# Kernel tuning notes

Hardware: AMD Instinct MI355X
Metric: run time of the kernel (lower is better)

The kernel has to match this reference:

```python
import jax, jax.numpy as jnp
import numpy as np

FEATURE_LIST = [10, 13, 13, 7, 3, 6, 3, 13, 5, 4, 6, 4, 5, 4, 4, 5, 4, 3, 3, 7, 3, 3]
BATCH = 1048576
D_IN = sum(FEATURE_LIST)  # 128


def setup_inputs() -> dict:
    key = jax.random.key(0)
    k1, k2, k3 = jax.random.split(key, 3)
    x = jax.random.normal(k1, (BATCH, D_IN), dtype=jnp.float32)
    # per-block kernels (fn, 1) packed along axis 0 into (128, 1); 'uniform' init
    kernels = jax.random.uniform(k2, (D_IN, 1), dtype=jnp.float32, minval=-0.05, maxval=0.05)
    biases = jnp.zeros((len(FEATURE_LIST),), dtype=jnp.float32)
    final_kernel = jax.random.uniform(k3, (len(FEATURE_LIST), 1), dtype=jnp.float32, minval=-0.05, maxval=0.05)
    final_bias = jnp.zeros((1,), dtype=jnp.float32)
    return {"x": x, "kernels": kernels, "biases": biases,
            "final_kernel": final_kernel, "final_bias": final_bias}


def reference(x, kernels, biases, final_kernel, final_bias):
    nodes = []
    off = 0
    start_i = 0  # NOTE: original TF code never increments start_i -> every block reads x[:, 0:fn]
    for i, fn in enumerate(FEATURE_LIST):
        k = kernels[off:off + fn]                      # (fn, 1)
        node = jax.nn.relu(x[:, start_i:start_i + fn] @ k + biases[i])  # (B, 1)
        nodes.append(node)
        off += fn
    h = jnp.concatenate(nodes, axis=1)                 # (B, 22)
    return jax.nn.sigmoid(h @ final_kernel + final_bias)  # (B, 1)
```

## Files before the change

### kernel.cpp

```cpp
#include <hip/hip_runtime.h>
#include <math.h>

#define NFEAT 22
#define ROWS_PER_THREAD 2
#define BLOCK 256


__global__ __launch_bounds__(BLOCK, 8) void hnn_fused_kernel(
    const float* __restrict__ x,
    const float* __restrict__ kernels,
    const float* __restrict__ biases,
    const float* __restrict__ final_kernel,
    const float* __restrict__ final_bias,
    float* __restrict__ out,
    int batch)
{
    constexpr int FN[NFEAT] = {10,13,13,7,3,6,3,13,5,4,6,4,5,4,4,5,4,3,3,7,3,3};

    const int base = blockIdx.x * (BLOCK * ROWS_PER_THREAD) + threadIdx.x;

    #pragma unroll
    for (int r = 0; r < ROWS_PER_THREAD; ++r) {
        const int row = base + r * BLOCK;
        if (row >= batch) continue;

        const size_t rb = (size_t)row * 128;
        const float4* xr = reinterpret_cast<const float4*>(x + rb);

        float4 a = xr[0];
        float4 b = xr[1];
        float4 c = xr[2];
        float xv[13] = {a.x, a.y, a.z, a.w,
                        b.x, b.y, b.z, b.w,
                        c.x, c.y, c.z, c.w,
                        x[rb + 12]};

        float z = final_bias[0];
        int off = 0;
        #pragma unroll
        for (int i = 0; i < NFEAT; ++i) {
            float acc = biases[i];
            #pragma unroll
            for (int j = 0; j < FN[i]; ++j) {
                acc = fmaf(xv[j], kernels[off + j], acc);
            }
            off += FN[i];
            z = fmaf(fmaxf(acc, 0.0f), final_kernel[i], z);
        }

        out[row] = 1.0f / (1.0f + __expf(-z));
    }
}

extern "C" void kernel_launch(void* const* d_in, const int* in_sizes, int n_in,
                              void* d_out, int out_size, void* d_ws, size_t ws_size,
                              hipStream_t stream)
{
    const float* x            = (const float*)d_in[0];
    const float* kernels      = (const float*)d_in[1];
    const float* biases       = (const float*)d_in[2];
    const float* final_kernel = (const float*)d_in[3];
    const float* final_bias   = (const float*)d_in[4];
    float* out = (float*)d_out;

    const int batch = out_size;
    const int rows_per_block = BLOCK * ROWS_PER_THREAD;
    const int grid = (batch + rows_per_block - 1) / rows_per_block;

    hnn_fused_kernel<<<grid, BLOCK, 0, stream>>>(
        x, kernels, biases, final_kernel, final_bias, out, batch);
}
```

Measured before the change: 26.62 us.

## Stage input rows through swizzled LDS with coalesced cooperative loads

Four threads now cooperatively load the first 64 bytes of each row as float4s into shared memory, using an XOR swizzle to avoid bank conflicts. After a barrier, each thread reads its own row back from LDS and computes. The aim is to replace strided per-thread global loads with coalesced ones. In exchange it adds LDS traffic and a block barrier, and each thread now handles one row instead of two.

Result: slower. 31.20 us (+17.2%).

```diff
diff --git a/kernel.cpp b/kernel.cpp
--- a/kernel.cpp
+++ b/kernel.cpp
@@ -2,8 +2,8 @@
 #include <math.h>
 
 #define NFEAT 22
-#define ROWS_PER_THREAD 2
 #define BLOCK 256
+#define ROWS_PER_BLOCK 256
 
 
 __global__ __launch_bounds__(BLOCK, 8) void hnn_fused_kernel(
@@ -17,39 +17,58 @@
 {
     constexpr int FN[NFEAT] = {10,13,13,7,3,6,3,13,5,4,6,4,5,4,4,5,4,3,3,7,3,3};
 
-    const int base = blockIdx.x * (BLOCK * ROWS_PER_THREAD) + threadIdx.x;
+    __shared__ float lds[ROWS_PER_BLOCK * 16];
 
+    const int t = threadIdx.x;
+    const int rowBase = blockIdx.x * ROWS_PER_BLOCK;
+
+    {
+        const int c    = t & 3;
+        const int rloc = t >> 2;
+        const int swz  = (t >> 3) & 3;
+        const int ce   = c ^ swz;
+        #pragma unroll
+        for (int k = 0; k < 4; ++k) {
+            const int rr    = rloc + 64 * k;
+            const int row_g = rowBase + rr;
+            if (row_g < batch) {
+                const float4 v = *reinterpret_cast<const float4*>(
+                    x + (size_t)row_g * 128 + c * 4);
+                *reinterpret_cast<float4*>(&lds[rr * 16 + ce * 4]) = v;
+            }
+        }
+    }
+    __syncthreads();
+
+    const int row = rowBase + t;
+    if (row >= batch) return;
+
+    const int rs = (t >> 1) & 3;
+    float4 q[4];
     #pragma unroll
-    for (int r = 0; r < ROWS_PER_THREAD; ++r) {
-        const int row = base + r * BLOCK;
-        if (row >= batch) continue;
+    for (int cc = 0; cc < 4; ++cc) {
+        const int ce = cc ^ rs;
+        q[cc] = *reinterpret_cast<const float4*>(&lds[t * 16 + ce * 4]);
+    }
+    const float xv[13] = {q[0].x, q[0].y, q[0].z, q[0].w,
+                          q[1].x, q[1].y, q[1].z, q[1].w,
+                          q[2].x, q[2].y, q[2].z, q[2].w,
+                          q[3].x};
 
-        const size_t rb = (size_t)row * 128;
-        const float4* xr = reinterpret_cast<const float4*>(x + rb);
+    float z = final_bias[0];
+    int off = 0;
+    #pragma unroll
+    for (int i = 0; i < NFEAT; ++i) {
+        float acc = biases[i];
+        #pragma unroll
+        for (int j = 0; j < FN[i]; ++j) {
+            acc = fmaf(xv[j], kernels[off + j], acc);
+        }
+        off += FN[i];
+        z = fmaf(fmaxf(acc, 0.0f), final_kernel[i], z);
+    }
 
-        float4 a = xr[0];
-        float4 b = xr[1];
-        float4 c = xr[2];
-        float xv[13] = {a.x, a.y, a.z, a.w,
-                        b.x, b.y, b.z, b.w,
-                        c.x, c.y, c.z, c.w,
-                        x[rb + 12]};
-
-        float z = final_bias[0];
-        int off = 0;
-        #pragma unroll
-        for (int i = 0; i < NFEAT; ++i) {
-            float acc = biases[i];
-            #pragma unroll
-            for (int j = 0; j < FN[i]; ++j) {
-                acc = fmaf(xv[j], kernels[off + j], acc);
-            }
-            off += FN[i];
-            z = fmaf(fmaxf(acc, 0.0f), final_kernel[i], z);
-        }
-
-        out[row] = 1.0f / (1.0f + __expf(-z));
-    }
+    out[row] = 1.0f / (1.0f + __expf(-z));
 }
 
 extern "C" void kernel_launch(void* const* d_in, const int* in_sizes, int n_in,
@@ -64,8 +83,7 @@
     float* out = (float*)d_out;
 
     const int batch = out_size;
-    const int rows_per_block = BLOCK * ROWS_PER_THREAD;
-    const int grid = (batch + rows_per_block - 1) / rows_per_block;
+    const int grid = (batch + ROWS_PER_BLOCK - 1) / ROWS_PER_BLOCK;
 
     hnn_fused_kernel<<<grid, BLOCK, 0, stream>>>(
         x, kernels, biases, final_kernel, final_bias, out, batch);
```
